# Optimization experiments

Hardware: AMD Instinct MI355X
Metric: run time of the kernel (lower is better)

The kernel has to match this reference:

```python
import math
import jax, jax.numpy as jnp
import numpy as np

L, D, H, DF, V, T, B = 4, 1024, 16, 4096, 32000, 2048, 1
HD = D // H
EPS = 1e-5

def _ln(x, w, b):
    m = jnp.mean(x, -1, keepdims=True)
    v = jnp.mean((x - m) ** 2, -1, keepdims=True)
    return (x - m) * jax.lax.rsqrt(v + EPS) * w + b

def setup_inputs() -> dict:
    key = jax.random.key(0)
    ks = jax.random.split(key, 8)
    s = 0.02
    return {
        'ids':   jax.random.randint(ks[0], (B, T), 0, V),
        'te':    jax.random.normal(ks[1], (V, D), jnp.float32) * s,
        'pe':    jax.random.normal(ks[2], (T, D), jnp.float32) * s,
        'qkv_w': jax.random.normal(ks[3], (L, D, 3 * D), jnp.float32) * s,
        'qkv_b': jnp.zeros((L, 3 * D), jnp.float32),
        'out_w': jax.random.normal(ks[4], (L, D, D), jnp.float32) * s,
        'out_b': jnp.zeros((L, D), jnp.float32),
        'ln1_w': jnp.ones((L, D), jnp.float32),
        'ln1_b': jnp.zeros((L, D), jnp.float32),
        'ln2_w': jnp.ones((L, D), jnp.float32),
        'ln2_b': jnp.zeros((L, D), jnp.float32),
        'up_w':  jax.random.normal(ks[5], (L, D, DF), jnp.float32) * s,
        'up_b':  jnp.zeros((L, DF), jnp.float32),
        'dn_w':  jax.random.normal(ks[6], (L, DF, D), jnp.float32) * s,
        'dn_b':  jnp.zeros((L, D), jnp.float32),
        'lnf_w': jnp.ones((D,), jnp.float32),
        'lnf_b': jnp.zeros((D,), jnp.float32),
    }

def reference(ids, te, pe, qkv_w, qkv_b, out_w, out_b, ln1_w, ln1_b,
              ln2_w, ln2_b, up_w, up_b, dn_w, dn_b, lnf_w, lnf_b):
    b, t = ids.shape
    x = te[ids] + pe[:t][None]                        # [b,t,D]
    causal = jnp.tril(jnp.ones((t, t), bool))          # [t,t]
    scale = 1.0 / math.sqrt(HD)
    for i in range(L):
        h = _ln(x, ln1_w[i], ln1_b[i])
        qkv = (h @ qkv_w[i] + qkv_b[i]).reshape(b, t, 3, H, HD)
        q, k, v = qkv[:, :, 0], qkv[:, :, 1], qkv[:, :, 2]
        sc = jnp.einsum('bqhd,bkhd->bhqk', q, k) * scale
        sc = jnp.where(causal, sc, -jnp.inf)
        att = jax.nn.softmax(sc, axis=-1)
        ao = jnp.einsum('bhqk,bkhd->bqhd', att, v).reshape(b, t, D)
        x = x + ao @ out_w[i] + out_b[i]
        h = _ln(x, ln2_w[i], ln2_b[i])
        x = x + jax.nn.silu(h @ up_w[i] + up_b[i]) @ dn_w[i] + dn_b[i]
    x = _ln(x, lnf_w, lnf_b)
    logits = x @ te.T                                  # tied head, no bias
    return logits
```

## Files before the change

### kernel.cpp

```cpp
#include <hip/hip_runtime.h>

typedef __attribute__((ext_vector_type(8))) short short8;
typedef __attribute__((ext_vector_type(4))) short short4v;
typedef __attribute__((ext_vector_type(4))) float f32x4;
typedef unsigned short u16;

#define Lc 4
#define Dc 1024
#define Hc 16
#define HDc 64
#define DFc 4096
#define Vc 32000
#define Tc 2048

__device__ __forceinline__ u16 f2bf(float f) {
  union { float f; unsigned u; } v; v.f = f;
  return (u16)((v.u + 0x7FFFu + ((v.u >> 16) & 1u)) >> 16);
}

__device__ __forceinline__ void gload_lds16(const u16* g, u16* l) {
  __builtin_amdgcn_global_load_lds(
      (const __attribute__((address_space(1))) unsigned int*)(g),
      (__attribute__((address_space(3))) unsigned int*)(l), 16, 0, 0);
}

#define BARS do { __builtin_amdgcn_s_barrier(); __builtin_amdgcn_sched_barrier(0); } while (0)
#define LGKM(n) do { asm volatile("s_waitcnt lgkmcnt(" #n ")" ::: "memory"); __builtin_amdgcn_sched_barrier(0); } while (0)
#define VMC(n) do { asm volatile("s_waitcnt vmcnt(" #n ")" ::: "memory"); __builtin_amdgcn_sched_barrier(0); } while (0)

__global__ __launch_bounds__(256) void castk(const float* __restrict__ in, u16* __restrict__ out) {
  size_t i = ((size_t)blockIdx.x * 256 + threadIdx.x) * 4;
  float4 v = *(const float4*)(in + i);
  short4v o; o[0] = f2bf(v.x); o[1] = f2bf(v.y); o[2] = f2bf(v.z); o[3] = f2bf(v.w);
  *(short4v*)(out + i) = o;
}

__global__ __launch_bounds__(256) void embedln(const int* __restrict__ ids, const float* __restrict__ te,
                                               const float* __restrict__ pe, const float* __restrict__ w,
                                               const float* __restrict__ b, float* __restrict__ x,
                                               u16* __restrict__ out) {
  int t = blockIdx.x, tid = threadIdx.x;
  int id = ids[t];
  float4 a = *(const float4*)(te + (size_t)id * Dc + tid * 4);
  float4 p = *(const float4*)(pe + (size_t)t * Dc + tid * 4);
  float4 v; v.x = a.x + p.x; v.y = a.y + p.y; v.z = a.z + p.z; v.w = a.w + p.w;
  size_t i = (size_t)t * Dc + tid * 4;
  *(float4*)(x + i) = v;
  float s = v.x + v.y + v.z + v.w;
  float q = v.x * v.x + v.y * v.y + v.z * v.z + v.w * v.w;
  #pragma unroll
  for (int off = 1; off < 64; off <<= 1) { s += __shfl_xor(s, off); q += __shfl_xor(q, off); }
  __shared__ float red[8];
  if ((tid & 63) == 0) { red[tid >> 6] = s; red[4 + (tid >> 6)] = q; }
  __syncthreads();
  s = red[0] + red[1] + red[2] + red[3];
  q = red[4] + red[5] + red[6] + red[7];
  float mean = s * (1.0f / Dc);
  float rstd = rsqrtf(q * (1.0f / Dc) - mean * mean + 1e-5f);
  float4 wv = *(const float4*)(w + tid * 4);
  float4 bv = *(const float4*)(b + tid * 4);
  out[i + 0] = f2bf((v.x - mean) * rstd * wv.x + bv.x);
  out[i + 1] = f2bf((v.y - mean) * rstd * wv.y + bv.y);
  out[i + 2] = f2bf((v.z - mean) * rstd * wv.z + bv.z);
  out[i + 3] = f2bf((v.w - mean) * rstd * wv.w + bv.w);
}

template<int SK>
__global__ __launch_bounds__(256) void combineln(float* __restrict__ x, const float* __restrict__ p,
                                                 const float* __restrict__ bias, const float* __restrict__ w,
                                                 const float* __restrict__ b, u16* __restrict__ out) {
  int t = blockIdx.x, tid = threadIdx.x;
  size_t i = (size_t)t * Dc + tid * 4;
  float4 v = *(const float4*)(x + i);
  #pragma unroll
  for (int s = 0; s < SK; s++) {
    float4 q2 = *(const float4*)(p + (size_t)s * Tc * Dc + i);
    v.x += q2.x; v.y += q2.y; v.z += q2.z; v.w += q2.w;
  }
  float4 bb = *(const float4*)(bias + tid * 4);
  v.x += bb.x; v.y += bb.y; v.z += bb.z; v.w += bb.w;
  *(float4*)(x + i) = v;
  float s = v.x + v.y + v.z + v.w;
  float q = v.x * v.x + v.y * v.y + v.z * v.z + v.w * v.w;
  #pragma unroll
  for (int off = 1; off < 64; off <<= 1) { s += __shfl_xor(s, off); q += __shfl_xor(q, off); }
  __shared__ float red[8];
  if ((tid & 63) == 0) { red[tid >> 6] = s; red[4 + (tid >> 6)] = q; }
  __syncthreads();
  s = red[0] + red[1] + red[2] + red[3];
  q = red[4] + red[5] + red[6] + red[7];
  float mean = s * (1.0f / Dc);
  float rstd = rsqrtf(q * (1.0f / Dc) - mean * mean + 1e-5f);
  float4 wv = *(const float4*)(w + tid * 4);
  float4 bv = *(const float4*)(b + tid * 4);
  out[i + 0] = f2bf((v.x - mean) * rstd * wv.x + bv.x);
  out[i + 1] = f2bf((v.y - mean) * rstd * wv.y + bv.y);
  out[i + 2] = f2bf((v.z - mean) * rstd * wv.z + bv.z);
  out[i + 3] = f2bf((v.w - mean) * rstd * wv.w + bv.w);
}

__global__ __launch_bounds__(256) void transpose4(const float* __restrict__ qw, const float* __restrict__ ow,
                                                  const float* __restrict__ uw, const float* __restrict__ dw,
                                                  u16* __restrict__ qT, u16* __restrict__ oT,
                                                  u16* __restrict__ uT, u16* __restrict__ dT) {
  __shared__ float tl[32][33];
  int id = blockIdx.x;
  const float* in; u16* out; int R, C, t;
  if (id < 3072)      { in = qw; out = qT; R = Dc;  C = 3 * Dc; t = id; }
  else if (id < 4096) { in = ow; out = oT; R = Dc;  C = Dc;     t = id - 3072; }
  else if (id < 8192) { in = uw; out = uT; R = Dc;  C = DFc;    t = id - 4096; }
  else                { in = dw; out = dT; R = DFc; C = Dc;     t = id - 8192; }
  int tilesX = C >> 5;
  int c0 = (t % tilesX) * 32, r0 = (t / tilesX) * 32;
  int lx = threadIdx.x & 31, ly = threadIdx.x >> 5;
  #pragma unroll
  for (int i = ly; i < 32; i += 8) tl[i][lx] = in[(size_t)(r0 + i) * C + c0 + lx];
  __syncthreads();
  #pragma unroll
  for (int i = ly; i < 32; i += 8) out[(size_t)(c0 + i) * R + r0 + lx] = f2bf(tl[lx][i]);
}

template<int EPI>
__global__ __launch_bounds__(256) void gemm128m(
    const u16* __restrict__ A, const u16* __restrict__ Bt, const float* __restrict__ bias,
    u16* __restrict__ outb, float* __restrict__ outf, int M, int N, int K, int KS) {
  __shared__ __align__(16) u16 lds[32768];
  u16* As = lds;
  u16* Bs = lds + 16384;
  const int NK = KS >> 6;

  int tid = threadIdx.x;
  int w = tid >> 6, lane = tid & 63;
  int lr = lane & 15, lg = lane >> 4;
  int wr = w >> 1, wc = w & 1;

  int m0 = blockIdx.y * 128, n0 = blockIdx.x * 128;
  int kbase = blockIdx.z * KS;

  int offg[4];
  #pragma unroll
  for (int j = 0; j < 4; j++) {
    int p = tid + j * 256;
    int row = p >> 3;
    int uc = (p & 7) ^ (row & 7);
    offg[j] = row * K + uc * 8;
  }
  const u16* aB = A + (size_t)m0 * K + kbase;
  const u16* bB = Bt + (size_t)n0 * K + kbase;

  auto stA = [&](int kt) {
    u16* l = As + ((kt & 1) << 13) + w * 512;
    #pragma unroll
    for (int j = 0; j < 4; j++)
      gload_lds16(aB + kt * 64 + offg[j], l + j * 2048);
  };
  auto stB = [&](int kt) {
    u16* l = Bs + ((kt & 1) << 13) + w * 512;
    #pragma unroll
    for (int j = 0; j < 4; j++)
      gload_lds16(bB + kt * 64 + offg[j], l + j * 2048);
  };

  int colx0 = ((0 * 4 + lg) ^ (lr & 7)) * 8;
  int colx1 = ((1 * 4 + lg) ^ (lr & 7)) * 8;
  int abase = (wr * 64 + lr) * 64;
  int bbase = (wc * 64 + lr) * 64;

  f32x4 acc[4][4] = {};

  stB(0); stA(0); stB(1);
  VMC(4);
  BARS;

  for (int kt = 0; kt < NK; ++kt) {
    const u16* sA = As + ((kt & 1) << 13);
    const u16* sB = Bs + ((kt & 1) << 13);
    short8 af[4][2], bf[4][2];

    #pragma unroll
    for (int m = 0; m < 2; m++) {
      af[m][0] = *(const short8*)(sA + abase + m * 1024 + colx0);
      af[m][1] = *(const short8*)(sA + abase + m * 1024 + colx1);
    }
    #pragma unroll
    for (int n = 0; n < 4; n++) {
      bf[n][0] = *(const short8*)(sB + bbase + n * 1024 + colx0);
      bf[n][1] = *(const short8*)(sB + bbase + n * 1024 + colx1);
    }
    if (kt + 1 < NK) stA(kt + 1);
    BARS;
    LGKM(0);
    __builtin_amdgcn_s_setprio(1);
    #pragma unroll
    for (int m = 0; m < 2; m++)
      #pragma unroll
      for (int n = 0; n < 4; n++)
        #pragma unroll
        for (int ks = 0; ks < 2; ks++)
          acc[m][n] = __builtin_amdgcn_mfma_f32_16x16x32_bf16(af[m][ks], bf[n][ks], acc[m][n], 0, 0, 0);
    __builtin_amdgcn_s_setprio(0);
    BARS;

    #pragma unroll
    for (int m = 2; m < 4; m++) {
      af[m][0] = *(const short8*)(sA + abase + m * 1024 + colx0);
      af[m][1] = *(const short8*)(sA + abase + m * 1024 + colx1);
    }
    if (kt + 2 < NK) { stB(kt + 2); VMC(4); }
    else if (kt + 1 < NK) { VMC(0); }
    BARS;
    LGKM(0);
    __builtin_amdgcn_s_setprio(1);
    #pragma unroll
    for (int m = 2; m < 4; m++)
      #pragma unroll
      for (int n = 0; n < 4; n++)
        #pragma unroll
        for (int ks = 0; ks < 2; ks++)
          acc[m][n] = __builtin_amdgcn_mfma_f32_16x16x32_bf16(af[m][ks], bf[n][ks], acc[m][n], 0, 0, 0);
    __builtin_amdgcn_s_setprio(0);
    BARS;
  }

  float* op = outf + (EPI == 4 ? (size_t)blockIdx.z * M * N : 0);
  u16* vtp = (u16*)outf;
  #pragma unroll
  for (int n = 0; n < 4; n++) {
    int gn = n0 + wc * 64 + n * 16 + lr;
    float bv = (EPI == 0 || EPI == 1 || EPI == 5) ? bias[gn] : 0.0f;
    #pragma unroll
    for (int m = 0; m < 4; m++) {
      if (EPI == 5 && gn >= 2 * Dc) {
        int gmb = m0 + wr * 64 + m * 16 + lg * 4;
        short4v o;
        #pragma unroll
        for (int r = 0; r < 4; r++) o[r] = (short)f2bf(acc[m][n][r] + bv);
        *(short4v*)(vtp + (size_t)(gn - 2 * Dc) * Tc + gmb) = o;
      } else {
        #pragma unroll
        for (int r = 0; r < 4; r++) {
          int gm = m0 + wr * 64 + m * 16 + lg * 4 + r;
          float v = acc[m][n][r] + bv;
          size_t idx = (size_t)gm * N + gn;
          if (EPI == 0 || EPI == 5) outb[idx] = f2bf(v);
          else if (EPI == 1) outb[idx] = f2bf(v / (1.0f + __expf(-v)));
          else op[idx] = v;
        }
      }
    }
  }
}

__global__ __launch_bounds__(512) void gemm256(const u16* __restrict__ A, const u16* __restrict__ Bt,
                                               float* __restrict__ outf, int M, int N, int K) {
  __shared__ __align__(16) u16 lds[65536];
  u16* AsU = lds;
  u16* BsU = lds + 32768;
  const int NK = K >> 6;

  int tid = threadIdx.x;
  int w = tid >> 6, lane = tid & 63;
  int lr = lane & 15, lg = lane >> 4;
  int wr = w >> 2, wc = w & 3;

  int flat = blockIdx.y * gridDim.x + blockIdx.x;
  {
    int nwg = gridDim.x * gridDim.y;
    int q = nwg >> 3, r = nwg & 7, xc = flat & 7, s = flat >> 3;
    flat = (xc < r ? xc * (q + 1) : r * (q + 1) + (xc - r) * q) + s;
  }
  int bm = flat % gridDim.x, bn = flat / gridDim.x;
  int m0 = bm * 256, n0 = bn * 256;

  int row0 = tid >> 3;
  int uc0 = (tid & 7) ^ (row0 & 7);
  int offg = row0 * K + uc0 * 8;
  const u16* aB = A + (size_t)m0 * K;
  const u16* bB = Bt + (size_t)n0 * K;

  auto stA = [&](int kt, int half) {
    const u16* g = aB + (size_t)half * 128 * K + kt * 64 + offg;
    u16* l = AsU + (((kt & 1) * 2 + half) << 13) + w * 512;
    gload_lds16(g, l);
    gload_lds16(g + 64 * K, l + 4096);
  };
  auto stB = [&](int kt, int half) {
    const u16* g = bB + (size_t)half * 128 * K + kt * 64 + offg;
    u16* l = BsU + (((kt & 1) * 2 + half) << 13) + w * 512;
    gload_lds16(g, l);
    gload_lds16(g + 64 * K, l + 4096);
  };

  int colx0 = ((0 * 4 + lg) ^ (lr & 7)) * 8;
  int colx1 = ((1 * 4 + lg) ^ (lr & 7)) * 8;
  int arow = lr * 64;
  int brow = ((wc & 1) * 64 + lr) * 64;

  short8 af0[4][2], af1[4][2], bf0[2][2], bf1[2][2];

  auto rd_af_lo = [&](int slot) {
    const u16* sA = AsU + ((slot * 2 + wr) << 13);
    #pragma unroll
    for (int m = 0; m < 4; m++) {
      af0[m][0] = *(const short8*)(sA + arow + m * 1024 + colx0);
      af0[m][1] = *(const short8*)(sA + arow + m * 1024 + colx1);
    }
  };
  auto rd_af_hi = [&](int slot) {
    const u16* sA = AsU + ((slot * 2 + wr) << 13);
    #pragma unroll
    for (int m = 0; m < 4; m++) {
      af1[m][0] = *(const short8*)(sA + arow + (m + 4) * 1024 + colx0);
      af1[m][1] = *(const short8*)(sA + arow + (m + 4) * 1024 + colx1);
    }
  };
  auto rd_bf = [&](int slot) {
    const u16* sB = BsU + ((slot * 2 + (wc >> 1)) << 13);
    #pragma unroll
    for (int n = 0; n < 2; n++) {
      bf0[n][0] = *(const short8*)(sB + brow + n * 1024 + colx0);
      bf0[n][1] = *(const short8*)(sB + brow + n * 1024 + colx1);
      bf1[n][0] = *(const short8*)(sB + brow + (n + 2) * 1024 + colx0);
      bf1[n][1] = *(const short8*)(sB + brow + (n + 2) * 1024 + colx1);
    }
  };

  f32x4 acc[8][4] = {};

  stB(0, 0); stB(0, 1); stA(0, 0); stA(0, 1); stB(1, 0); stB(1, 1);
  VMC(4);
  BARS;
  rd_af_lo(0);

  for (int kt = 0; kt < NK; ++kt) {
    int slot = kt & 1;
    rd_bf(slot);
    rd_af_hi(slot);
    LGKM(8);
    BARS;
    if (kt + 1 < NK) { stA(kt + 1, 0); stA(kt + 1, 1); }
    __builtin_amdgcn_s_setprio(1);
    #pragma unroll
    for (int m = 0; m < 4; m++)
      #pragma unroll
      for (int n = 0; n < 2; n++)
        #pragma unroll
        for (int ks = 0; ks < 2; ks++)
          acc[m][n] = __builtin_amdgcn_mfma_f32_16x16x32_bf16(af0[m][ks], bf0[n][ks], acc[m][n], 0, 0, 0);
    #pragma unroll
    for (int m = 0; m < 4; m++)
      #pragma unroll
      for (int n = 0; n < 2; n++)
        #pragma unroll
        for (int ks = 0; ks < 2; ks++)
          acc[m][n + 2] = __builtin_amdgcn_mfma_f32_16x16x32_bf16(af0[m][ks], bf1[n][ks], acc[m][n + 2], 0, 0, 0);
    __builtin_amdgcn_s_setprio(0);
    if (kt + 2 < NK) { stB(kt + 2, 0); stB(kt + 2, 1); VMC(4); }
    else if (kt + 1 < NK) { VMC(0); }
    BARS;
    if (kt + 1 < NK) {
      rd_af_lo((kt + 1) & 1);
      LGKM(8);
    } else {
      LGKM(0);
    }
    __builtin_amdgcn_s_setprio(1);
    #pragma unroll
    for (int m = 0; m < 4; m++)
      #pragma unroll
      for (int n = 0; n < 2; n++)
        #pragma unroll
        for (int ks = 0; ks < 2; ks++)
          acc[m + 4][n] = __builtin_amdgcn_mfma_f32_16x16x32_bf16(af1[m][ks], bf0[n][ks], acc[m + 4][n], 0, 0, 0);
    #pragma unroll
    for (int m = 0; m < 4; m++)
      #pragma unroll
      for (int n = 0; n < 2; n++)
        #pragma unroll
        for (int ks = 0; ks < 2; ks++)
          acc[m + 4][n + 2] = __builtin_amdgcn_mfma_f32_16x16x32_bf16(af1[m][ks], bf1[n][ks], acc[m + 4][n + 2], 0, 0, 0);
    __builtin_amdgcn_s_setprio(0);
  }

  {
    float* lf = (float*)lds;
    #pragma unroll
    for (int pass = 0; pass < 2; pass++) {
      BARS;
      if (wr == pass) {
        #pragma unroll
        for (int n = 0; n < 4; n++) {
          int col = wc * 64 + n * 16 + lr;
          #pragma unroll
          for (int m = 0; m < 8; m++)
            #pragma unroll
            for (int r = 0; r < 4; r++) {
              int rl = m * 16 + lg * 4 + r;
              lf[rl * 256 + (col ^ (((rl >> 2) & 1) << 4))] = acc[m][n][r];
            }
        }
      }
      BARS;
      #pragma unroll
      for (int j = 0; j < 16; j++) {
        int i4 = j * 2048 + tid * 4;
        int row = i4 >> 8;
        int col4 = i4 & 255;
        f32x4 v = *(const f32x4*)(lf + row * 256 + (col4 ^ (((row >> 2) & 1) << 4)));
        *(f32x4*)(outf + (size_t)(m0 + pass * 128 + row) * N + n0 + col4) = v;
      }
    }
  }
}

__global__ __launch_bounds__(512) void attnk(const u16* __restrict__ qkv, const u16* __restrict__ vt,
                                             u16* __restrict__ ao) {
  __shared__ u16 Plds[8][16][72];
  __shared__ float Cacc[4][64][16];
  __shared__ float Cl[4][64][4];
  int bid = blockIdx.x;
  int hh = bid >> 5;
  int qb = (bid & 256) ? (31 - (bid & 31)) : (bid & 31);
  int tid = threadIdx.x, l = tid & 63, w = tid >> 6;
  int w4 = w & 3, ishi = w >> 2;
  int lr = l & 15, lg = l >> 4;
  int qr0 = qb * 64 + w4 * 16;
  const u16* qbase = qkv + (size_t)(qr0 + lr) * (3 * Dc) + hh * HDc + lg * 8;
  short8 aq0 = *(const short8*)qbase;
  short8 aq1 = *(const short8*)(qbase + 32);
  f32x4 acco[4] = {};
  float rs[4] = {0.0f, 0.0f, 0.0f, 0.0f};
  int nkb = (qr0 + 79) >> 6;
  int half = nkb >> 1;
  int klo = ishi ? half : 0;
  int khi = ishi ? nkb : half;
  const float cl2 = 0.125f * 1.44269504088896f;
  for (int kb = klo; kb < khi; kb++) {
    int kk0 = kb * 64;
    float sv[4][4];
    bool msk = (kb == nkb - 1);
    #pragma unroll
    for (int st = 0; st < 4; st++) {
      int kt0 = kk0 + st * 16;
      const u16* kbase = qkv + (size_t)(kt0 + lr) * (3 * Dc) + Dc + hh * HDc + lg * 8;
      short8 bk0 = *(const short8*)kbase;
      short8 bk1 = *(const short8*)(kbase + 32);
      f32x4 s = {};
      s = __builtin_amdgcn_mfma_f32_16x16x32_bf16(aq0, bk0, s, 0, 0, 0);
      s = __builtin_amdgcn_mfma_f32_16x16x32_bf16(aq1, bk1, s, 0, 0, 0);
      if (msk) {
        int gcol = kt0 + lr;
        #pragma unroll
        for (int r = 0; r < 4; r++) {
          int grow = qr0 + lg * 4 + r;
          sv[st][r] = (gcol <= grow) ? s[r] * cl2 : -__builtin_inff();
        }
      } else {
        #pragma unroll
        for (int r = 0; r < 4; r++) sv[st][r] = s[r] * cl2;
      }
    }
    #pragma unroll
    for (int st = 0; st < 4; st++) {
      #pragma unroll
      for (int r = 0; r < 4; r++) {
        float p = __builtin_amdgcn_exp2f(fminf(sv[st][r], 45.0f));
        sv[st][r] = p;
        rs[r] += p;
      }
    }
    #pragma unroll
    for (int st = 0; st < 4; st++) {
      #pragma unroll
      for (int r = 0; r < 4; r++) Plds[w][lg * 4 + r][st * 16 + lr] = f2bf(sv[st][r]);
    }
    short8 pa0 = *(const short8*)&Plds[w][lr][lg * 8];
    short8 pa1 = *(const short8*)&Plds[w][lr][32 + lg * 8];
    #pragma unroll
    for (int nt = 0; nt < 4; nt++) {
      const u16* vbase = vt + (size_t)(hh * HDc + nt * 16 + lr) * Tc + kk0 + lg * 8;
      short8 bv0 = *(const short8*)vbase;
      short8 bv1 = *(const short8*)(vbase + 32);
      acco[nt] = __builtin_amdgcn_mfma_f32_16x16x32_bf16(pa0, bv0, acco[nt], 0, 0, 0);
      acco[nt] = __builtin_amdgcn_mfma_f32_16x16x32_bf16(pa1, bv1, acco[nt], 0, 0, 0);
    }
  }
  #pragma unroll
  for (int off = 1; off < 16; off <<= 1) {
    #pragma unroll
    for (int r = 0; r < 4; r++) rs[r] += __shfl_xor(rs[r], off);
  }
  if (ishi) {
    #pragma unroll
    for (int nt = 0; nt < 4; nt++)
      #pragma unroll
      for (int r = 0; r < 4; r++) Cacc[w4][l][nt * 4 + r] = acco[nt][r];
    #pragma unroll
    for (int r = 0; r < 4; r++) Cl[w4][l][r] = rs[r];
  }
  __syncthreads();
  if (!ishi) {
    float linv[4];
    #pragma unroll
    for (int r = 0; r < 4; r++) linv[r] = 1.0f / (rs[r] + Cl[w4][l][r]);
    #pragma unroll
    for (int nt = 0; nt < 4; nt++) {
      #pragma unroll
      for (int r = 0; r < 4; r++) {
        float val = (acco[nt][r] + Cacc[w4][l][nt * 4 + r]) * linv[r];
        ao[(size_t)(qr0 + lg * 4 + r) * Dc + hh * HDc + nt * 16 + lr] = f2bf(val);
      }
    }
  }
}

extern "C" void kernel_launch(void* const* d_in, const int* in_sizes, int n_in,
                              void* d_out, int out_size, void* d_ws, size_t ws_size,
                              hipStream_t stream) {
  const int*   ids   = (const int*)d_in[0];
  const float* te    = (const float*)d_in[1];
  const float* pe    = (const float*)d_in[2];
  const float* qkv_w = (const float*)d_in[3];
  const float* qkv_b = (const float*)d_in[4];
  const float* out_w = (const float*)d_in[5];
  const float* out_b = (const float*)d_in[6];
  const float* ln1_w = (const float*)d_in[7];
  const float* ln1_b = (const float*)d_in[8];
  const float* ln2_w = (const float*)d_in[9];
  const float* ln2_b = (const float*)d_in[10];
  const float* up_w  = (const float*)d_in[11];
  const float* up_b  = (const float*)d_in[12];
  const float* dn_w  = (const float*)d_in[13];
  const float* dn_b  = (const float*)d_in[14];
  const float* lnf_w = (const float*)d_in[15];
  const float* lnf_b = (const float*)d_in[16];
  float* logits = (float*)d_out;

  char* ws = (char*)d_ws;
  size_t off = 0;
  auto alloc = [&](size_t bytes) { void* p = ws + off; off += (bytes + 255) & ~(size_t)255; return p; };
  float* x    = (float*)alloc((size_t)Tc * Dc * 4);
  u16* hbuf   = (u16*)alloc((size_t)Tc * Dc * 2);
  u16* qkvb   = (u16*)alloc((size_t)Tc * 3 * Dc * 2);
  u16* aob    = (u16*)alloc((size_t)Tc * Dc * 2);
  u16* ubuf   = (u16*)alloc((size_t)Tc * DFc * 2);
  u16* vtb    = (u16*)alloc((size_t)Dc * Tc * 2);
  u16* tebf   = (u16*)alloc((size_t)Vc * Dc * 2);
  u16* qkvT   = (u16*)alloc((size_t)3 * Dc * Dc * 2);
  u16* outT   = (u16*)alloc((size_t)Dc * Dc * 2);
  u16* upT    = (u16*)alloc((size_t)DFc * Dc * 2);
  u16* dnT    = (u16*)alloc((size_t)Dc * DFc * 2);
  float* pbuf = (float*)alloc((size_t)4 * Tc * Dc * 4);

  castk<<<Vc * Dc / 1024, 256, 0, stream>>>(te, tebf);
  embedln<<<Tc, 256, 0, stream>>>(ids, te, pe, ln1_w, ln1_b, x, hbuf);

  for (int i = 0; i < Lc; i++) {
    transpose4<<<12288, 256, 0, stream>>>(
        qkv_w + (size_t)i * Dc * 3 * Dc, out_w + (size_t)i * Dc * Dc,
        up_w + (size_t)i * Dc * DFc, dn_w + (size_t)i * DFc * Dc,
        qkvT, outT, upT, dnT);

    gemm128m<5><<<dim3(3 * Dc / 128, Tc / 128, 1), 256, 0, stream>>>(
        hbuf, qkvT, qkv_b + (size_t)i * 3 * Dc, qkvb, (float*)vtb, Tc, 3 * Dc, Dc, Dc);
    attnk<<<512, 512, 0, stream>>>(qkvb, vtb, aob);
    gemm128m<4><<<dim3(Dc / 128, Tc / 128, 2), 256, 0, stream>>>(
        aob, outT, nullptr, nullptr, pbuf, Tc, Dc, Dc, Dc / 2);
    combineln<2><<<Tc, 256, 0, stream>>>(x, pbuf, out_b + (size_t)i * Dc,
                                         ln2_w + (size_t)i * Dc, ln2_b + (size_t)i * Dc, hbuf);
    gemm128m<1><<<dim3(DFc / 128, Tc / 128, 1), 256, 0, stream>>>(
        hbuf, upT, up_b + (size_t)i * DFc, ubuf, nullptr, Tc, DFc, Dc, Dc);
    gemm128m<4><<<dim3(Dc / 128, Tc / 128, 4), 256, 0, stream>>>(
        ubuf, dnT, nullptr, nullptr, pbuf, Tc, Dc, DFc, DFc / 4);
    if (i < Lc - 1)
      combineln<4><<<Tc, 256, 0, stream>>>(x, pbuf, dn_b + (size_t)i * Dc,
                                           ln1_w + (size_t)(i + 1) * Dc, ln1_b + (size_t)(i + 1) * Dc, hbuf);
    else
      combineln<4><<<Tc, 256, 0, stream>>>(x, pbuf, dn_b + (size_t)i * Dc, lnf_w, lnf_b, hbuf);
  }

  gemm256<<<dim3(Tc / 256, Vc / 256), 512, 0, stream>>>(hbuf, tebf, logits, Tc, Vc, Dc);
}
```

Baseline: 933.2 us.

## Batch weight transposes into one launch, split V transpose, halve down-proj split-K

```diff
diff --git a/kernel.cpp b/kernel.cpp
--- a/kernel.cpp
+++ b/kernel.cpp
@@ -99,17 +99,18 @@
   out[i + 3] = f2bf((v.w - mean) * rstd * wv.w + bv.w);
 }
 
-__global__ __launch_bounds__(256) void transpose4(const float* __restrict__ qw, const float* __restrict__ ow,
-                                                  const float* __restrict__ uw, const float* __restrict__ dw,
-                                                  u16* __restrict__ qT, u16* __restrict__ oT,
-                                                  u16* __restrict__ uT, u16* __restrict__ dT) {
+__global__ __launch_bounds__(256) void transpose16(const float* __restrict__ qw, const float* __restrict__ ow,
+                                                   const float* __restrict__ uw, const float* __restrict__ dw,
+                                                   u16* __restrict__ qT, u16* __restrict__ oT,
+                                                   u16* __restrict__ uT, u16* __restrict__ dT) {
   __shared__ float tl[32][33];
-  int id = blockIdx.x;
+  int lay = blockIdx.x / 12288;
+  int id = blockIdx.x % 12288;
   const float* in; u16* out; int R, C, t;
-  if (id < 3072)      { in = qw; out = qT; R = Dc;  C = 3 * Dc; t = id; }
-  else if (id < 4096) { in = ow; out = oT; R = Dc;  C = Dc;     t = id - 3072; }
-  else if (id < 8192) { in = uw; out = uT; R = Dc;  C = DFc;    t = id - 4096; }
-  else                { in = dw; out = dT; R = DFc; C = Dc;     t = id - 8192; }
+  if (id < 3072)      { in = qw + (size_t)lay * Dc * 3 * Dc; out = qT + (size_t)lay * 3 * Dc * Dc; R = Dc;  C = 3 * Dc; t = id; }
+  else if (id < 4096) { in = ow + (size_t)lay * Dc * Dc;     out = oT + (size_t)lay * Dc * Dc;     R = Dc;  C = Dc;     t = id - 3072; }
+  else if (id < 8192) { in = uw + (size_t)lay * Dc * DFc;    out = uT + (size_t)lay * DFc * Dc;    R = Dc;  C = DFc;    t = id - 4096; }
+  else                { in = dw + (size_t)lay * DFc * Dc;    out = dT + (size_t)lay * Dc * DFc;    R = DFc; C = Dc;     t = id - 8192; }
   int tilesX = C >> 5;
   int c0 = (t % tilesX) * 32, r0 = (t / tilesX) * 32;
   int lx = threadIdx.x & 31, ly = threadIdx.x >> 5;
@@ -118,6 +119,20 @@
   __syncthreads();
   #pragma unroll
   for (int i = ly; i < 32; i += 8) out[(size_t)(c0 + i) * R + r0 + lx] = f2bf(tl[lx][i]);
+}
+
+__global__ __launch_bounds__(256) void transpose_v(const u16* __restrict__ qkv, u16* __restrict__ vt) {
+  __shared__ u16 tl[32][34];
+  int hh = blockIdx.z;
+  int t0 = blockIdx.y * 32, d0 = blockIdx.x * 32;
+  int lx = threadIdx.x & 31, ly = threadIdx.x >> 5;
+  #pragma unroll
+  for (int i = ly; i < 32; i += 8)
+    tl[i][lx] = qkv[(size_t)(t0 + i) * (3 * Dc) + 2 * Dc + hh * HDc + d0 + lx];
+  __syncthreads();
+  #pragma unroll
+  for (int i = ly; i < 32; i += 8)
+    vt[(size_t)(hh * HDc + d0 + i) * Tc + t0 + lx] = tl[lx][i];
 }
 
 template<int EPI>
@@ -223,29 +238,20 @@
   }
 
   float* op = outf + (EPI == 4 ? (size_t)blockIdx.z * M * N : 0);
-  u16* vtp = (u16*)outf;
   #pragma unroll
   for (int n = 0; n < 4; n++) {
     int gn = n0 + wc * 64 + n * 16 + lr;
-    float bv = (EPI == 0 || EPI == 1 || EPI == 5) ? bias[gn] : 0.0f;
+    float bv = (EPI == 0 || EPI == 1) ? bias[gn] : 0.0f;
     #pragma unroll
     for (int m = 0; m < 4; m++) {
-      if (EPI == 5 && gn >= 2 * Dc) {
-        int gmb = m0 + wr * 64 + m * 16 + lg * 4;
-        short4v o;
-        #pragma unroll
-        for (int r = 0; r < 4; r++) o[r] = (short)f2bf(acc[m][n][r] + bv);
-        *(short4v*)(vtp + (size_t)(gn - 2 * Dc) * Tc + gmb) = o;
-      } else {
-        #pragma unroll
-        for (int r = 0; r < 4; r++) {
-          int gm = m0 + wr * 64 + m * 16 + lg * 4 + r;
-          float v = acc[m][n][r] + bv;
-          size_t idx = (size_t)gm * N + gn;
-          if (EPI == 0 || EPI == 5) outb[idx] = f2bf(v);
-          else if (EPI == 1) outb[idx] = f2bf(v / (1.0f + __expf(-v)));
-          else op[idx] = v;
-        }
+      #pragma unroll
+      for (int r = 0; r < 4; r++) {
+        int gm = m0 + wr * 64 + m * 16 + lg * 4 + r;
+        float v = acc[m][n][r] + bv;
+        size_t idx = (size_t)gm * N + gn;
+        if (EPI == 0) outb[idx] = f2bf(v);
+        else if (EPI == 1) outb[idx] = f2bf(v / (1.0f + __expf(-v)));
+        else op[idx] = v;
       }
     }
   }
@@ -546,37 +552,34 @@
   u16* ubuf   = (u16*)alloc((size_t)Tc * DFc * 2);
   u16* vtb    = (u16*)alloc((size_t)Dc * Tc * 2);
   u16* tebf   = (u16*)alloc((size_t)Vc * Dc * 2);
-  u16* qkvT   = (u16*)alloc((size_t)3 * Dc * Dc * 2);
-  u16* outT   = (u16*)alloc((size_t)Dc * Dc * 2);
-  u16* upT    = (u16*)alloc((size_t)DFc * Dc * 2);
-  u16* dnT    = (u16*)alloc((size_t)Dc * DFc * 2);
-  float* pbuf = (float*)alloc((size_t)4 * Tc * Dc * 4);
+  u16* qkvT   = (u16*)alloc((size_t)Lc * 3 * Dc * Dc * 2);
+  u16* outT   = (u16*)alloc((size_t)Lc * Dc * Dc * 2);
+  u16* upT    = (u16*)alloc((size_t)Lc * DFc * Dc * 2);
+  u16* dnT    = (u16*)alloc((size_t)Lc * Dc * DFc * 2);
+  float* pbuf = (float*)alloc((size_t)2 * Tc * Dc * 4);
 
   castk<<<Vc * Dc / 1024, 256, 0, stream>>>(te, tebf);
+  transpose16<<<4 * 12288, 256, 0, stream>>>(qkv_w, out_w, up_w, dn_w, qkvT, outT, upT, dnT);
   embedln<<<Tc, 256, 0, stream>>>(ids, te, pe, ln1_w, ln1_b, x, hbuf);
 
   for (int i = 0; i < Lc; i++) {
-    transpose4<<<12288, 256, 0, stream>>>(
-        qkv_w + (size_t)i * Dc * 3 * Dc, out_w + (size_t)i * Dc * Dc,
-        up_w + (size_t)i * Dc * DFc, dn_w + (size_t)i * DFc * Dc,
-        qkvT, outT, upT, dnT);
-
-    gemm128m<5><<<dim3(3 * Dc / 128, Tc / 128, 1), 256, 0, stream>>>(
-        hbuf, qkvT, qkv_b + (size_t)i * 3 * Dc, qkvb, (float*)vtb, Tc, 3 * Dc, Dc, Dc);
+    gemm128m<0><<<dim3(3 * Dc / 128, Tc / 128, 1), 256, 0, stream>>>(
+        hbuf, qkvT + (size_t)i * 3 * Dc * Dc, qkv_b + (size_t)i * 3 * Dc, qkvb, nullptr, Tc, 3 * Dc, Dc, Dc);
+    transpose_v<<<dim3(2, Tc / 32, Hc), 256, 0, stream>>>(qkvb, vtb);
     attnk<<<512, 512, 0, stream>>>(qkvb, vtb, aob);
     gemm128m<4><<<dim3(Dc / 128, Tc / 128, 2), 256, 0, stream>>>(
-        aob, outT, nullptr, nullptr, pbuf, Tc, Dc, Dc, Dc / 2);
+        aob, outT + (size_t)i * Dc * Dc, nullptr, nullptr, pbuf, Tc, Dc, Dc, Dc / 2);
     combineln<2><<<Tc, 256, 0, stream>>>(x, pbuf, out_b + (size_t)i * Dc,
                                          ln2_w + (size_t)i * Dc, ln2_b + (size_t)i * Dc, hbuf);
     gemm128m<1><<<dim3(DFc / 128, Tc / 128, 1), 256, 0, stream>>>(
-        hbuf, upT, up_b + (size_t)i * DFc, ubuf, nullptr, Tc, DFc, Dc, Dc);
-    gemm128m<4><<<dim3(Dc / 128, Tc / 128, 4), 256, 0, stream>>>(
-        ubuf, dnT, nullptr, nullptr, pbuf, Tc, Dc, DFc, DFc / 4);
+        hbuf, upT + (size_t)i * DFc * Dc, up_b + (size_t)i * DFc, ubuf, nullptr, Tc, DFc, Dc, Dc);
+    gemm128m<4><<<dim3(Dc / 128, Tc / 128, 2), 256, 0, stream>>>(
+        ubuf, dnT + (size_t)i * Dc * DFc, nullptr, nullptr, pbuf, Tc, Dc, DFc, DFc / 2);
     if (i < Lc - 1)
-      combineln<4><<<Tc, 256, 0, stream>>>(x, pbuf, dn_b + (size_t)i * Dc,
+      combineln<2><<<Tc, 256, 0, stream>>>(x, pbuf, dn_b + (size_t)i * Dc,
                                            ln1_w + (size_t)(i + 1) * Dc, ln1_b + (size_t)(i + 1) * Dc, hbuf);
     else
-      combineln<4><<<Tc, 256, 0, stream>>>(x, pbuf, dn_b + (size_t)i * Dc, lnf_w, lnf_b, hbuf);
+      combineln<2><<<Tc, 256, 0, stream>>>(x, pbuf, dn_b + (size_t)i * Dc, lnf_w, lnf_b, hbuf);
   }
 
   gemm256<<<dim3(Tc / 256, Vc / 256), 512, 0, stream>>>(hbuf, tebf, logits, Tc, Vc, Dc);
```

Result: no change. 945.9 us (+1.4%).
